# Kernel tuning notes

Measured on AMD Instinct MI355X. Metric: run time of the kernel, lower is better.

Reference implementation:

```python
import jax, jax.numpy as jnp
import numpy as np

H = 1024

def setup_inputs() -> dict:
    key = jax.random.key(0)
    k1, k2, k3, k4, k5 = jax.random.split(key, 5)
    B, T = 32, 2048
    s = 1.0 / np.sqrt(H)
    return {
        "decoder_state": jax.random.normal(k1, (B, H), dtype=jnp.float32),
        "encoder_states": jax.random.normal(k2, (B, T, H), dtype=jnp.float32),
        "Wa_w": jax.random.uniform(k3, (H, H), jnp.float32, -s, s),
        "Wa_b": jnp.zeros((H,), jnp.float32),
        "Ua_w": jax.random.uniform(k4, (H, H), jnp.float32, -s, s),
        "Ua_b": jnp.zeros((H,), jnp.float32),
        "v_w": jax.random.uniform(k5, (H,), jnp.float32, -s, s),
        "v_b": jnp.zeros((), jnp.float32),
    }

def reference(decoder_state, encoder_states, Wa_w, Wa_b, Ua_w, Ua_b, v_w, v_b):
    # decoder_state: [B,H], encoder_states: [B,T,H]
    dec_proj = decoder_state @ Ua_w.T + Ua_b            # [B,H]
    enc_proj = jnp.einsum('bth,oh->bto', encoder_states, Wa_w) + Wa_b  # [B,T,H]
    e = jnp.tanh(dec_proj[:, None, :] + enc_proj)        # [B,T,H]
    scores = jnp.einsum('bth,h->bt', e, v_w) + v_b       # [B,T]
    attn_weights = jax.nn.softmax(scores, axis=1)        # [B,T]
    context = jnp.einsum('bt,bth->bh', attn_weights, encoder_states)  # [B,H]
    return (context, attn_weights)
```

## Files before the change

### kernel.cpp

```cpp
#include <hip/hip_runtime.h>
#include <hip/hip_bf16.h>

#define HH 1024
#define BB 32
#define TT 2048

typedef __attribute__((ext_vector_type(8))) short bf16x8;
typedef __attribute__((ext_vector_type(4))) float f32x4;

static __device__ __forceinline__ unsigned short f2bf(float f) {
    unsigned int u = __float_as_uint(f);
    unsigned int r = u + 0x7fffu + ((u >> 16) & 1u);
    return (unsigned short)(r >> 16);
}
static __device__ __forceinline__ float bf2f(unsigned short u) {
    return __uint_as_float(((unsigned int)u) << 16);
}
static __device__ __forceinline__ float fast_tanh(float x) {
    float e = __expf(2.0f * x);
    return 1.0f - 2.0f / (e + 1.0f);
}

#define GLOAD_LDS16(gp, lp) \
    __builtin_amdgcn_global_load_lds( \
        (const __attribute__((address_space(1))) void*)(gp), \
        (__attribute__((address_space(3))) void*)(lp), 16, 0, 0)

__global__ void k_convW(const float* __restrict__ W, unsigned short* __restrict__ Wb) {
    int i = blockIdx.x * 256 + threadIdx.x;
    float4 v = ((const float4*)W)[i];
    ushort4 o;
    o.x = f2bf(v.x); o.y = f2bf(v.y); o.z = f2bf(v.z); o.w = f2bf(v.w);
    ((ushort4*)Wb)[i] = o;
}

__global__ void k_convEnc(const float* __restrict__ E, unsigned short* __restrict__ Eb) {
    long i = ((long)blockIdx.x * 256 + threadIdx.x) * 8;
    float4 a = *(const float4*)(E + i);
    float4 b = *(const float4*)(E + i + 4);
    ushort4 o0, o1;
    o0.x = f2bf(a.x); o0.y = f2bf(a.y); o0.z = f2bf(a.z); o0.w = f2bf(a.w);
    o1.x = f2bf(b.x); o1.y = f2bf(b.y); o1.z = f2bf(b.z); o1.w = f2bf(b.w);
    *(ushort4*)(Eb + i) = o0;
    *(ushort4*)(Eb + i + 4) = o1;
}

__global__ void k_decproj(const float* __restrict__ dec, const float* __restrict__ Ua,
                          const float* __restrict__ Uab, const float* __restrict__ Wab,
                          float* __restrict__ dp) {
    int gtid = blockIdx.x * 256 + threadIdx.x;
    int b = gtid >> 10, o = gtid & 1023;
    const float4* d4 = (const float4*)(dec + (long)b * HH);
    const float4* u4 = (const float4*)(Ua + (long)o * HH);
    float acc = 0.f;
    for (int k = 0; k < HH / 4; ++k) {
        float4 a = d4[k], w = u4[k];
        acc += a.x * w.x + a.y * w.y + a.z * w.z + a.w * w.w;
    }
    dp[gtid] = acc + Uab[o] + Wab[o];
}

__global__ __launch_bounds__(512) void k_score_bf(
        const unsigned short* __restrict__ encb, const unsigned short* __restrict__ Wb,
        const float* __restrict__ dp, const float* __restrict__ vw,
        float* __restrict__ scores) {
    __shared__ __align__(16) unsigned short As[2][256 * 64];
    __shared__ __align__(16) unsigned short Bs[2][256 * 64];
    int bid = blockIdx.x;
    int xcd = bid & 7;
    int ord = bid >> 3;
    int nt = ord & 3;
    int mt = (ord >> 2) * 8 + xcd;
    long m0 = (long)mt * 256;
    int o0b = nt * 256;
    int tid = threadIdx.x;
    int lane = tid & 63, wid = tid >> 6;
    int wm = wid >> 2, wn = wid & 3;
    int r = lane & 15, g = lane >> 4;

    f32x4 acc[8][4];
    #pragma unroll
    for (int i = 0; i < 8; ++i)
        #pragma unroll
        for (int j = 0; j < 4; ++j) acc[i][j] = (f32x4){0.f, 0.f, 0.f, 0.f};

    int srow = tid >> 3;
    int swu = (tid & 7) ^ (srow & 7);
    const unsigned short* aSrc = encb + (m0 + srow) * HH + swu * 8;
    const unsigned short* bSrc = Wb + (long)(o0b + srow) * HH + swu * 8;
    int ldso = wid * 512;
    int rx = r & 7;
    int u0 = (g ^ rx) * 8;
    int u1 = ((4 + g) ^ rx) * 8;

    #pragma unroll
    for (int p = 0; p < 4; ++p) {
        GLOAD_LDS16(aSrc + p * 64 * HH, &As[0][ldso + p * 4096]);
        GLOAD_LDS16(bSrc + p * 64 * HH, &Bs[0][ldso + p * 4096]);
    }
    __syncthreads();

    #pragma unroll 1
    for (int t = 0; t < 16; ++t) {
        const int bi = t & 1, pi = bi ^ 1;
        const int kc2 = (t + 1) * 64;
        const bool pre = (t < 15);
        bf16x8 bfr[4][2];

        #pragma unroll
        for (int p = 0; p < 4; ++p) {
            bf16x8 aqr[2][2];
            #pragma unroll
            for (int q = 0; q < 2; ++q) {
                int rowa = (wm * 128 + (2 * p + q) * 16 + r) * 64;
                aqr[q][0] = *(const bf16x8*)(&As[bi][rowa + u0]);
                aqr[q][1] = *(const bf16x8*)(&As[bi][rowa + u1]);
            }
            if (p == 0) {
                #pragma unroll
                for (int ni = 0; ni < 4; ++ni) {
                    int rowb = (wn * 64 + ni * 16 + r) * 64;
                    bfr[ni][0] = *(const bf16x8*)(&Bs[bi][rowb + u0]);
                    bfr[ni][1] = *(const bf16x8*)(&Bs[bi][rowb + u1]);
                }
            }
            if (pre && p == 0) {
                #pragma unroll
                for (int q = 0; q < 4; ++q)
                    GLOAD_LDS16(aSrc + kc2 + q * 64 * HH,
                                &As[pi][ldso + q * 4096]);
            }
            if (pre && p == 1) {
                #pragma unroll
                for (int q = 0; q < 4; ++q)
                    GLOAD_LDS16(bSrc + kc2 + q * 64 * HH,
                                &Bs[pi][ldso + q * 4096]);
            }
            __builtin_amdgcn_s_barrier();
            asm volatile("s_waitcnt lgkmcnt(0)" ::: "memory");
            __builtin_amdgcn_sched_barrier(0);
            __builtin_amdgcn_s_setprio(1);
            #pragma unroll
            for (int q = 0; q < 2; ++q) {
                int mi = 2 * p + q;
                #pragma unroll
                for (int ni = 0; ni < 4; ++ni) {
                    acc[mi][ni] = __builtin_amdgcn_mfma_f32_16x16x32_bf16(
                        aqr[q][0], bfr[ni][0], acc[mi][ni], 0, 0, 0);
                    acc[mi][ni] = __builtin_amdgcn_mfma_f32_16x16x32_bf16(
                        aqr[q][1], bfr[ni][1], acc[mi][ni], 0, 0, 0);
                }
            }
            __builtin_amdgcn_s_setprio(0);
            if (p == 3 && pre)
                asm volatile("s_waitcnt vmcnt(0)" ::: "memory");
            __builtin_amdgcn_s_barrier();
        }
    }

    int bb = (int)(m0 >> 11);
    float vv[4], dpv[4];
    #pragma unroll
    for (int ni = 0; ni < 4; ++ni) {
        int o = o0b + wn * 64 + ni * 16 + r;
        vv[ni] = vw[o];
        dpv[ni] = dp[bb * HH + o];
    }
    #pragma unroll
    for (int mi = 0; mi < 8; ++mi) {
        float vp[4] = {0.f, 0.f, 0.f, 0.f};
        #pragma unroll
        for (int ni = 0; ni < 4; ++ni)
            #pragma unroll
            for (int j = 0; j < 4; ++j)
                vp[j] += fast_tanh(acc[mi][ni][j] + dpv[ni]) * vv[ni];
        #pragma unroll
        for (int j = 0; j < 4; ++j) {
            float s = vp[j];
            s += __shfl_xor(s, 1); s += __shfl_xor(s, 2);
            s += __shfl_xor(s, 4); s += __shfl_xor(s, 8);
            if (r == 0) {
                int row = wm * 128 + mi * 16 + g * 4 + j;
                atomicAdd(&scores[m0 + row], s);
            }
        }
    }
}

#define LDSP 40
__global__ __launch_bounds__(256) void k_score(const float* __restrict__ enc,
        const unsigned short* __restrict__ Wb, const float* __restrict__ dp,
        const float* __restrict__ vw, float* __restrict__ scores) {
    __shared__ __align__(16) unsigned short As[128][LDSP];
    __shared__ __align__(16) unsigned short Bs[128][LDSP];
    int bid = blockIdx.x;
    int nt = bid & 7;
    int mt = bid >> 3;
    long m0 = (long)mt * 128;
    int o0 = nt * 128;
    int tid = threadIdx.x;
    int lane = tid & 63, wid = tid >> 6;
    int wm = wid >> 1, wn = wid & 1;
    int r = lane & 15, g = lane >> 4;

    f32x4 acc[4][4];
    #pragma unroll
    for (int i = 0; i < 4; ++i)
        #pragma unroll
        for (int j = 0; j < 4; ++j) acc[i][j] = (f32x4){0.f, 0.f, 0.f, 0.f};

    for (int kc = 0; kc < HH; kc += 32) {
        #pragma unroll
        for (int i = 0; i < 4; ++i) {
            int idx = tid + i * 256;
            int row = idx >> 3, kq = idx & 7;
            float4 a = *(const float4*)(enc + (m0 + row) * HH + kc + kq * 4);
            ushort4 p;
            p.x = f2bf(a.x); p.y = f2bf(a.y); p.z = f2bf(a.z); p.w = f2bf(a.w);
            *(ushort4*)(&As[row][kq * 4]) = p;
        }
        #pragma unroll
        for (int i = 0; i < 2; ++i) {
            int idx = tid + i * 256;
            int row = idx >> 2, kq = idx & 3;
            *(int4*)(&Bs[row][kq * 8]) =
                *(const int4*)(Wb + (long)(o0 + row) * HH + kc + kq * 8);
        }
        __syncthreads();
        bf16x8 af[4], bfr[4];
        #pragma unroll
        for (int mi = 0; mi < 4; ++mi)
            af[mi] = *(const bf16x8*)(&As[wm * 64 + mi * 16 + r][g * 8]);
        #pragma unroll
        for (int ni = 0; ni < 4; ++ni)
            bfr[ni] = *(const bf16x8*)(&Bs[wn * 64 + ni * 16 + r][g * 8]);
        #pragma unroll
        for (int mi = 0; mi < 4; ++mi)
            #pragma unroll
            for (int ni = 0; ni < 4; ++ni)
                acc[mi][ni] = __builtin_amdgcn_mfma_f32_16x16x32_bf16(
                    af[mi], bfr[ni], acc[mi][ni], 0, 0, 0);
        __syncthreads();
    }

    int bb = (int)(m0 >> 11);
    #pragma unroll
    for (int mi = 0; mi < 4; ++mi) {
        float vp[4] = {0.f, 0.f, 0.f, 0.f};
        #pragma unroll
        for (int ni = 0; ni < 4; ++ni) {
            int o = o0 + wn * 64 + ni * 16 + r;
            float vvs = vw[o];
            float dpvs = dp[bb * HH + o];
            #pragma unroll
            for (int j = 0; j < 4; ++j)
                vp[j] += fast_tanh(acc[mi][ni][j] + dpvs) * vvs;
        }
        #pragma unroll
        for (int j = 0; j < 4; ++j) {
            float s = vp[j];
            s += __shfl_xor(s, 1); s += __shfl_xor(s, 2);
            s += __shfl_xor(s, 4); s += __shfl_xor(s, 8);
            if (r == 0) {
                int row = wm * 64 + mi * 16 + g * 4 + j;
                atomicAdd(&scores[m0 + row], s);
            }
        }
    }
}

__global__ void k_softmax(float* __restrict__ w) {
    int b = blockIdx.x;
    float* row = w + (long)b * TT;
    int tid = threadIdx.x;
    float loc[8];
    float m = -1e30f;
    #pragma unroll
    for (int i = 0; i < 8; ++i) { loc[i] = row[tid + i * 256]; m = fmaxf(m, loc[i]); }
    #pragma unroll
    for (int off = 1; off < 64; off <<= 1) m = fmaxf(m, __shfl_xor(m, off));
    __shared__ float red[4];
    if ((tid & 63) == 0) red[tid >> 6] = m;
    __syncthreads();
    m = fmaxf(fmaxf(red[0], red[1]), fmaxf(red[2], red[3]));
    float s = 0.f;
    #pragma unroll
    for (int i = 0; i < 8; ++i) { loc[i] = __expf(loc[i] - m); s += loc[i]; }
    #pragma unroll
    for (int off = 1; off < 64; off <<= 1) s += __shfl_xor(s, off);
    __shared__ float red2[4];
    if ((tid & 63) == 0) red2[tid >> 6] = s;
    __syncthreads();
    s = red2[0] + red2[1] + red2[2] + red2[3];
    float inv = 1.0f / s;
    #pragma unroll
    for (int i = 0; i < 8; ++i) row[tid + i * 256] = loc[i] * inv;
}

__global__ void k_context_bf(const unsigned short* __restrict__ encb,
                             const float* __restrict__ w, float* __restrict__ ctx) {
    int bid = blockIdx.x;
    int b = bid >> 4;
    int ts = bid & 15;
    int h = threadIdx.x * 4;
    const float* wr = w + (long)b * TT + ts * 128;
    long base = ((long)b * TT + (long)ts * 128) * HH + h;
    float a0 = 0.f, a1 = 0.f, a2 = 0.f, a3 = 0.f;
    #pragma unroll 4
    for (int t = 0; t < 128; ++t) {
        ushort4 e = *(const ushort4*)(encb + base + (long)t * HH);
        float ww = wr[t];
        a0 += ww * bf2f(e.x);
        a1 += ww * bf2f(e.y);
        a2 += ww * bf2f(e.z);
        a3 += ww * bf2f(e.w);
    }
    atomicAdd(&ctx[b * HH + h], a0);
    atomicAdd(&ctx[b * HH + h + 1], a1);
    atomicAdd(&ctx[b * HH + h + 2], a2);
    atomicAdd(&ctx[b * HH + h + 3], a3);
}

__global__ void k_context(const float* __restrict__ enc, const float* __restrict__ w,
                          float* __restrict__ ctx) {
    int bid = blockIdx.x;
    int b = bid >> 6;
    int hc = (bid >> 4) & 3;
    int ts = bid & 15;
    int h = hc * 256 + threadIdx.x;
    const float* wr = w + (long)b * TT + ts * 128;
    long base = ((long)b * TT + (long)ts * 128) * HH + h;
    float acc = 0.f;
    for (int t = 0; t < 128; ++t)
        acc += wr[t] * enc[base + (long)t * HH];
    atomicAdd(&ctx[b * HH + h], acc);
}

extern "C" void kernel_launch(void* const* d_in, const int* in_sizes, int n_in,
                              void* d_out, int out_size, void* d_ws, size_t ws_size,
                              hipStream_t stream) {
    const float* dec  = (const float*)d_in[0];
    const float* enc  = (const float*)d_in[1];
    const float* Wa_w = (const float*)d_in[2];
    const float* Wa_b = (const float*)d_in[3];
    const float* Ua_w = (const float*)d_in[4];
    const float* Ua_b = (const float*)d_in[5];
    const float* v_w  = (const float*)d_in[6];

    float* out  = (float*)d_out;
    float* ctx  = out;
    float* attn = out + BB * HH;

    float* dpw = (float*)d_ws;
    unsigned short* Wb = (unsigned short*)((char*)d_ws + 131072);
    unsigned short* encb = (unsigned short*)((char*)d_ws + 131072 + 2097152);
    const size_t NEED = 131072ull + 2097152ull + (size_t)BB * TT * HH * 2;

    hipMemsetAsync(d_out, 0, (size_t)out_size * sizeof(float), stream);
    k_convW<<<1024, 256, 0, stream>>>(Wa_w, Wb);
    k_decproj<<<128, 256, 0, stream>>>(dec, Ua_w, Ua_b, Wa_b, dpw);

    if (ws_size >= NEED) {
        k_convEnc<<<32768, 256, 0, stream>>>(enc, encb);
        k_score_bf<<<1024, 512, 0, stream>>>(encb, Wb, dpw, v_w, attn);
        k_softmax<<<BB, 256, 0, stream>>>(attn);
        k_context_bf<<<512, 256, 0, stream>>>(encb, attn, ctx);
    } else {
        k_score<<<4096, 256, 0, stream>>>(enc, Wb, dpw, v_w, attn);
        k_softmax<<<BB, 256, 0, stream>>>(attn);
        k_context<<<2048, 256, 0, stream>>>(enc, attn, ctx);
    }
}
```

Before: 299.6 us.

## Restructure GEMM main loop into four quadrant phases with split prefetch

Reorganizes the bf16 MFMA main loop into four quadrant-wise compute phases (A low/high halves × B column halves). Next-tile global→LDS loads are split into pairs issued between phases, gated by fine-grained vmcnt waits instead of a single full drain. The B tile's LDS row layout is permuted so each wave's column slices sit in separate 4096-element chunks. The aim is finer overlap of memory loads with MFMA and smaller waits per barrier. The cost is more barriers per iteration and fragile hand-tuned vmcnt counting.

```diff
diff --git a/kernel.cpp b/kernel.cpp
--- a/kernel.cpp
+++ b/kernel.cpp
@@ -87,75 +87,135 @@
     int srow = tid >> 3;
     int swu = (tid & 7) ^ (srow & 7);
     const unsigned short* aSrc = encb + (m0 + srow) * HH + swu * 8;
-    const unsigned short* bSrc = Wb + (long)(o0b + srow) * HH + swu * 8;
+    const unsigned short* bSrc =
+        Wb + (long)(o0b + 64 * (srow >> 4) + (srow & 15)) * HH + swu * 8;
     int ldso = wid * 512;
     int rx = r & 7;
     int u0 = (g ^ rx) * 8;
     int u1 = ((4 + g) ^ rx) * 8;
 
     #pragma unroll
-    for (int p = 0; p < 4; ++p) {
-        GLOAD_LDS16(aSrc + p * 64 * HH, &As[0][ldso + p * 4096]);
-        GLOAD_LDS16(bSrc + p * 64 * HH, &Bs[0][ldso + p * 4096]);
+    for (int q = 0; q < 4; ++q) {
+        GLOAD_LDS16(aSrc + q * 64 * HH, &As[0][ldso + q * 4096]);
+        GLOAD_LDS16(bSrc + (long)q * 16 * HH, &Bs[0][q * 4096 + ldso]);
     }
     __syncthreads();
 
     #pragma unroll 1
     for (int t = 0; t < 16; ++t) {
-        const int bi = t & 1, pi = bi ^ 1;
-        const int kc2 = (t + 1) * 64;
-        const bool pre = (t < 15);
-        bf16x8 bfr[4][2];
-
-        #pragma unroll
-        for (int p = 0; p < 4; ++p) {
-            bf16x8 aqr[2][2];
-            #pragma unroll
-            for (int q = 0; q < 2; ++q) {
-                int rowa = (wm * 128 + (2 * p + q) * 16 + r) * 64;
-                aqr[q][0] = *(const bf16x8*)(&As[bi][rowa + u0]);
-                aqr[q][1] = *(const bf16x8*)(&As[bi][rowa + u1]);
-            }
-            if (p == 0) {
-                #pragma unroll
-                for (int ni = 0; ni < 4; ++ni) {
-                    int rowb = (wn * 64 + ni * 16 + r) * 64;
-                    bfr[ni][0] = *(const bf16x8*)(&Bs[bi][rowb + u0]);
-                    bfr[ni][1] = *(const bf16x8*)(&Bs[bi][rowb + u1]);
-                }
-            }
-            if (pre && p == 0) {
-                #pragma unroll
-                for (int q = 0; q < 4; ++q)
-                    GLOAD_LDS16(aSrc + kc2 + q * 64 * HH,
-                                &As[pi][ldso + q * 4096]);
-            }
-            if (pre && p == 1) {
-                #pragma unroll
-                for (int q = 0; q < 4; ++q)
-                    GLOAD_LDS16(bSrc + kc2 + q * 64 * HH,
-                                &Bs[pi][ldso + q * 4096]);
-            }
-            __builtin_amdgcn_s_barrier();
-            asm volatile("s_waitcnt lgkmcnt(0)" ::: "memory");
-            __builtin_amdgcn_sched_barrier(0);
-            __builtin_amdgcn_s_setprio(1);
-            #pragma unroll
-            for (int q = 0; q < 2; ++q) {
-                int mi = 2 * p + q;
-                #pragma unroll
-                for (int ni = 0; ni < 4; ++ni) {
-                    acc[mi][ni] = __builtin_amdgcn_mfma_f32_16x16x32_bf16(
-                        aqr[q][0], bfr[ni][0], acc[mi][ni], 0, 0, 0);
-                    acc[mi][ni] = __builtin_amdgcn_mfma_f32_16x16x32_bf16(
-                        aqr[q][1], bfr[ni][1], acc[mi][ni], 0, 0, 0);
-                }
-            }
-            __builtin_amdgcn_s_setprio(0);
-            if (p == 3 && pre)
-                asm volatile("s_waitcnt vmcnt(0)" ::: "memory");
-            __builtin_amdgcn_s_barrier();
-        }
+        int bi = t & 1, pi = bi ^ 1;
+        int kc2 = (t + 1) * 64;
+        bool pre = (t < 15);
+        bf16x8 aLo[4][2], aHi[4][2], bfr[4][2];
+
+        if (pre) {
+            GLOAD_LDS16(aSrc + kc2 + 0 * 64 * HH, &As[pi][ldso + 0 * 4096]);
+            GLOAD_LDS16(aSrc + kc2 + 2 * 64 * HH, &As[pi][ldso + 2 * 4096]);
+            asm volatile("s_waitcnt vmcnt(6)" ::: "memory");
+        } else {
+            asm volatile("s_waitcnt vmcnt(4)" ::: "memory");
+        }
+        __builtin_amdgcn_s_barrier();
+        #pragma unroll
+        for (int mi = 0; mi < 4; ++mi) {
+            int rowa = (wm * 128 + mi * 16 + r) * 64;
+            aLo[mi][0] = *(const bf16x8*)(&As[bi][rowa + u0]);
+            aLo[mi][1] = *(const bf16x8*)(&As[bi][rowa + u1]);
+        }
+        #pragma unroll
+        for (int ni = 0; ni < 2; ++ni) {
+            int rowb = ni * 4096 + (wn * 16 + r) * 64;
+            bfr[ni][0] = *(const bf16x8*)(&Bs[bi][rowb + u0]);
+            bfr[ni][1] = *(const bf16x8*)(&Bs[bi][rowb + u1]);
+        }
+        asm volatile("s_waitcnt lgkmcnt(0)" ::: "memory");
+        __builtin_amdgcn_sched_barrier(0);
+        __builtin_amdgcn_s_setprio(1);
+        #pragma unroll
+        for (int mi = 0; mi < 4; ++mi)
+            #pragma unroll
+            for (int ni = 0; ni < 2; ++ni) {
+                acc[mi][ni] = __builtin_amdgcn_mfma_f32_16x16x32_bf16(
+                    aLo[mi][0], bfr[ni][0], acc[mi][ni], 0, 0, 0);
+                acc[mi][ni] = __builtin_amdgcn_mfma_f32_16x16x32_bf16(
+                    aLo[mi][1], bfr[ni][1], acc[mi][ni], 0, 0, 0);
+            }
+        __builtin_amdgcn_s_setprio(0);
+        __builtin_amdgcn_s_barrier();
+
+        if (pre) {
+            GLOAD_LDS16(bSrc + kc2 + (long)0 * 16 * HH, &Bs[pi][0 * 4096 + ldso]);
+            GLOAD_LDS16(bSrc + kc2 + (long)1 * 16 * HH, &Bs[pi][1 * 4096 + ldso]);
+            asm volatile("s_waitcnt vmcnt(6)" ::: "memory");
+        } else {
+            asm volatile("s_waitcnt vmcnt(2)" ::: "memory");
+        }
+        __builtin_amdgcn_s_barrier();
+        #pragma unroll
+        for (int ni = 2; ni < 4; ++ni) {
+            int rowb = ni * 4096 + (wn * 16 + r) * 64;
+            bfr[ni][0] = *(const bf16x8*)(&Bs[bi][rowb + u0]);
+            bfr[ni][1] = *(const bf16x8*)(&Bs[bi][rowb + u1]);
+        }
+        asm volatile("s_waitcnt lgkmcnt(0)" ::: "memory");
+        __builtin_amdgcn_sched_barrier(0);
+        __builtin_amdgcn_s_setprio(1);
+        #pragma unroll
+        for (int mi = 0; mi < 4; ++mi)
+            #pragma unroll
+            for (int ni = 2; ni < 4; ++ni) {
+                acc[mi][ni] = __builtin_amdgcn_mfma_f32_16x16x32_bf16(
+                    aLo[mi][0], bfr[ni][0], acc[mi][ni], 0, 0, 0);
+                acc[mi][ni] = __builtin_amdgcn_mfma_f32_16x16x32_bf16(
+                    aLo[mi][1], bfr[ni][1], acc[mi][ni], 0, 0, 0);
+            }
+        __builtin_amdgcn_s_setprio(0);
+        __builtin_amdgcn_s_barrier();
+
+        if (pre) {
+            GLOAD_LDS16(bSrc + kc2 + (long)2 * 16 * HH, &Bs[pi][2 * 4096 + ldso]);
+            GLOAD_LDS16(bSrc + kc2 + (long)3 * 16 * HH, &Bs[pi][3 * 4096 + ldso]);
+            asm volatile("s_waitcnt vmcnt(6)" ::: "memory");
+        } else {
+            asm volatile("s_waitcnt vmcnt(0)" ::: "memory");
+        }
+        __builtin_amdgcn_s_barrier();
+        #pragma unroll
+        for (int mi = 0; mi < 4; ++mi) {
+            int rowa = (wm * 128 + (mi + 4) * 16 + r) * 64;
+            aHi[mi][0] = *(const bf16x8*)(&As[bi][rowa + u0]);
+            aHi[mi][1] = *(const bf16x8*)(&As[bi][rowa + u1]);
+        }
+        asm volatile("s_waitcnt lgkmcnt(0)" ::: "memory");
+        __builtin_amdgcn_sched_barrier(0);
+        __builtin_amdgcn_s_setprio(1);
+        #pragma unroll
+        for (int mi = 0; mi < 4; ++mi)
+            #pragma unroll
+            for (int ni = 0; ni < 2; ++ni) {
+                acc[mi + 4][ni] = __builtin_amdgcn_mfma_f32_16x16x32_bf16(
+                    aHi[mi][0], bfr[ni][0], acc[mi + 4][ni], 0, 0, 0);
+                acc[mi + 4][ni] = __builtin_amdgcn_mfma_f32_16x16x32_bf16(
+                    aHi[mi][1], bfr[ni][1], acc[mi + 4][ni], 0, 0, 0);
+            }
+        __builtin_amdgcn_s_setprio(0);
+        __builtin_amdgcn_s_barrier();
+
+        if (pre) {
+            GLOAD_LDS16(aSrc + kc2 + 1 * 64 * HH, &As[pi][ldso + 1 * 4096]);
+            GLOAD_LDS16(aSrc + kc2 + 3 * 64 * HH, &As[pi][ldso + 3 * 4096]);
+        }
+        __builtin_amdgcn_s_setprio(1);
+        #pragma unroll
+        for (int mi = 0; mi < 4; ++mi)
+            #pragma unroll
+            for (int ni = 2; ni < 4; ++ni) {
+                acc[mi + 4][ni] = __builtin_amdgcn_mfma_f32_16x16x32_bf16(
+                    aHi[mi][0], bfr[ni][0], acc[mi + 4][ni], 0, 0, 0);
+                acc[mi + 4][ni] = __builtin_amdgcn_mfma_f32_16x16x32_bf16(
+                    aHi[mi][1], bfr[ni][1], acc[mi + 4][ni], 0, 0, 0);
+            }
+        __builtin_amdgcn_s_setprio(0);
     }
 
     int bb = (int)(m0 >> 11);
```

New measurement: 319.5 us. 6.7% more time.
